# Performance work log

Measured on AMD Instinct MI355X. Metric: run time of the kernel, lower is better.

## Reference

```python
import jax, jax.numpy as jnp
import numpy as np

DIM = 2048
HEADS = 16
HEAD_DIM = 128
KV_HEADS = 8
ROPE_BASE = 10000.0


def _rope_tables(seq_len):
    inv_freq = 1.0 / (ROPE_BASE ** (jnp.arange(0, HEAD_DIM, 2, dtype=jnp.float32) / HEAD_DIM))
    t = jnp.arange(seq_len, dtype=jnp.float32)
    freqs = jnp.outer(t, inv_freq)              # [S, D/2]
    emb = jnp.concatenate([freqs, freqs], -1)    # [S, D]
    return jnp.cos(emb), jnp.sin(emb)


def _rotate_half(x):
    x1, x2 = jnp.split(x, 2, axis=-1)
    return jnp.concatenate([-x2, x1], axis=-1)


def setup_inputs() -> dict:
    key = jax.random.key(0)
    ks = jax.random.split(key, 5)
    B, S = 2, 2048
    s = 0.02
    return {
        "x": jax.random.normal(ks[0], (B, S, DIM), jnp.float32),
        "Wq": jax.random.normal(ks[1], (DIM, HEADS * HEAD_DIM), jnp.float32) * s,
        "Wk": jax.random.normal(ks[2], (DIM, KV_HEADS * HEAD_DIM), jnp.float32) * s,
        "Wv": jax.random.normal(ks[3], (DIM, KV_HEADS * HEAD_DIM), jnp.float32) * s,
        "Wo": jax.random.normal(ks[4], (HEADS * HEAD_DIM, DIM), jnp.float32) * s,
    }


def reference(x, Wq, Wk, Wv, Wo):
    B, S, _ = x.shape
    scale = 1.0 / np.sqrt(HEAD_DIM).astype(np.float32)
    q = (x @ Wq).reshape(B, S, HEADS, HEAD_DIM)
    k = (x @ Wk).reshape(B, S, KV_HEADS, HEAD_DIM)
    v = (x @ Wv).reshape(B, S, KV_HEADS, HEAD_DIM)
    cos, sin = _rope_tables(S)                   # [S, D]
    cos = cos[None, :, None, :]                  # broadcast over batch, heads
    sin = sin[None, :, None, :]
    q = q * cos + _rotate_half(q) * sin
    k = k * cos + _rotate_half(k) * sin
    q = jnp.transpose(q, (0, 2, 1, 3))           # [B,H,S,D]
    k = jnp.transpose(k, (0, 2, 1, 3))           # [B,Hkv,S,D]
    v = jnp.transpose(v, (0, 2, 1, 3))
    rep = HEADS // KV_HEADS
    k = jnp.repeat(k, rep, axis=1)               # GQA -> [B,H,S,D]
    v = jnp.repeat(v, rep, axis=1)
    scores = jnp.einsum('bhid,bhjd->bhij', q, k) * scale
    causal = jnp.tril(jnp.ones((S, S), dtype=bool))
    scores = jnp.where(causal, scores, -jnp.inf)
    attn = jax.nn.softmax(scores, axis=-1)
    out = jnp.einsum('bhij,bhjd->bhid', attn, v)
    out = jnp.transpose(out, (0, 2, 1, 3)).reshape(B, S, HEADS * HEAD_DIM)
    return out @ Wo
```

## Files before the change

### kernel.cpp

```cpp
#include <hip/hip_runtime.h>

#define DIMX 2048
#define SEQ  2048
#define BATCH 2
#define NH   16
#define NKV  8
#define HD   128
#define MTOK (BATCH*SEQ)
#define NQKV 4096
#define QKLD 3072

typedef __bf16 bf16x8 __attribute__((ext_vector_type(8)));
typedef float  f32x4  __attribute__((ext_vector_type(4)));
typedef float  f32x16 __attribute__((ext_vector_type(16)));
typedef unsigned short u16x8 __attribute__((ext_vector_type(8)));
typedef unsigned short u16x4 __attribute__((ext_vector_type(4)));
typedef unsigned int   u32x4 __attribute__((ext_vector_type(4)));

__device__ __forceinline__ unsigned short f2bf(float f) {
    unsigned u = __builtin_bit_cast(unsigned, f);
    u += 0x7fffu + ((u >> 16) & 1u);
    return (unsigned short)(u >> 16);
}
__device__ __forceinline__ float bf2f(unsigned short h) {
    unsigned u = ((unsigned)h) << 16;
    return __builtin_bit_cast(float, u);
}

__device__ __forceinline__ void gload16(const void* g, void* l) {
    __builtin_amdgcn_global_load_lds(
        (const __attribute__((address_space(1))) unsigned int*)g,
        (__attribute__((address_space(3))) unsigned int*)l, 16, 0, 0);
}

__global__ __launch_bounds__(256) void k_convert(const float* __restrict__ in,
                                                 unsigned short* __restrict__ out, int n8) {
    int i = blockIdx.x * 256 + threadIdx.x;
    if (i >= n8) return;
    f32x4 a = ((const f32x4*)in)[(size_t)i*2];
    f32x4 b = ((const f32x4*)in)[(size_t)i*2+1];
    u16x8 o;
    o[0]=f2bf(a[0]); o[1]=f2bf(a[1]); o[2]=f2bf(a[2]); o[3]=f2bf(a[3]);
    o[4]=f2bf(b[0]); o[5]=f2bf(b[1]); o[6]=f2bf(b[2]); o[7]=f2bf(b[3]);
    ((u16x8*)out)[i] = o;
}

__global__ __launch_bounds__(256) void k_transpose(const float* __restrict__ W,
                                                   unsigned short* __restrict__ Wt,
                                                   int K, int N) {
    __shared__ unsigned short tile[64*65];
    int t = threadIdx.x;
    int n0 = blockIdx.x * 64, k0 = blockIdx.y * 64;
    #pragma unroll
    for (int i = 0; i < 16; ++i) {
        int idx = t + i*256, r = idx >> 6, c = idx & 63;
        tile[r*65+c] = f2bf(W[(size_t)(k0+r)*N + n0 + c]);
    }
    __syncthreads();
    #pragma unroll
    for (int i = 0; i < 16; ++i) {
        int idx = t + i*256, n = idx >> 6, k = idx & 63;
        Wt[(size_t)(n0+n)*K + k0 + k] = tile[k*65+n];
    }
}

template<int NREP, int MODE>
__global__ __launch_bounds__(512, 2) void k_gemm256(const unsigned short* __restrict__ A,
                                                    const unsigned short* __restrict__ Bt,
                                                    void* __restrict__ Cv,
                                                    unsigned short* __restrict__ Vt,
                                                    int M, int N, int K, int ldc) {
    constexpr int BN  = NREP * 64;
    constexpr int BWC = NREP * 16;
    __shared__ __align__(16) char As[2][32768];
    __shared__ __align__(16) char Bs[2][BN * 128];
    int bid = blockIdx.x;
    int rem = (bid & 7) * 32 + (bid >> 3);
    int bx = rem & 15, by = rem >> 4;
    int row0 = by * 256, col0 = bx * BN;
    int tid = threadIdx.x, wave = tid >> 6, lane = tid & 63;
    int wr = wave >> 2, wc = wave & 3;
    int g = lane >> 4, r16 = lane & 15;
    const char* Ab = (const char*)A;
    const char* Bb = (const char*)Bt;

    f32x4 acc[8][NREP] = {};

    auto STAGE = [&](int buf, int t) {
        int k0b = t * 128;
        #pragma unroll
        for (int p = 0; p < 4; ++p) {
            int c = wave * 4 + p;
            int o = c * 1024 + lane * 16;
            int row = o >> 7;
            int colb = (o & 127) ^ ((row & 7) << 4);
            gload16(Ab + (size_t)(row0 + row) * (size_t)(K * 2) + k0b + colb, &As[buf][c * 1024]);
        }
        #pragma unroll
        for (int p = 0; p < NREP; ++p) {
            int c = wave * NREP + p;
            int o = c * 1024 + lane * 16;
            int row = o >> 7;
            int colb = (o & 127) ^ ((row & 7) << 4);
            gload16(Bb + (size_t)(col0 + row) * (size_t)(K * 2) + k0b + colb, &Bs[buf][c * 1024]);
        }
    };

    int nt = K >> 6;
    STAGE(0, 0);
    STAGE(1, 1);
    if constexpr (NREP == 4) asm volatile("s_waitcnt vmcnt(8)" ::: "memory");
    else                     asm volatile("s_waitcnt vmcnt(6)" ::: "memory");
    __builtin_amdgcn_s_barrier();

    for (int t = 0; t < nt; ++t) {
        int buf = t & 1;
        const char* AL = As[buf];
        const char* BL = Bs[buf];
        bf16x8 a0[4][2], a1[4][2], bfr[NREP][2];
        #pragma unroll
        for (int mi = 0; mi < 4; ++mi)
            #pragma unroll
            for (int s = 0; s < 2; ++s) {
                int r = wr*128 + mi*16 + r16;
                int o = r*128 + s*64 + g*16;
                a0[mi][s] = *(const bf16x8*)(AL + (o ^ ((r & 7) << 4)));
            }
        #pragma unroll
        for (int ni = 0; ni < NREP; ++ni)
            #pragma unroll
            for (int s = 0; s < 2; ++s) {
                int r = wc*BWC + ni*16 + r16;
                int o = r*128 + s*64 + g*16;
                bfr[ni][s] = *(const bf16x8*)(BL + (o ^ ((r & 7) << 4)));
            }
        __builtin_amdgcn_s_setprio(1);
        #pragma unroll
        for (int mi = 0; mi < 4; ++mi)
            #pragma unroll
            for (int ni = 0; ni < NREP; ++ni)
                #pragma unroll
                for (int s = 0; s < 2; ++s)
                    acc[mi][ni] = __builtin_amdgcn_mfma_f32_16x16x32_bf16(a0[mi][s], bfr[ni][s], acc[mi][ni], 0, 0, 0);
        __builtin_amdgcn_s_setprio(0);
        #pragma unroll
        for (int mi = 0; mi < 4; ++mi)
            #pragma unroll
            for (int s = 0; s < 2; ++s) {
                int r = wr*128 + 64 + mi*16 + r16;
                int o = r*128 + s*64 + g*16;
                a1[mi][s] = *(const bf16x8*)(AL + (o ^ ((r & 7) << 4)));
            }
        asm volatile("s_waitcnt lgkmcnt(0)" ::: "memory");
        __builtin_amdgcn_sched_barrier(0);
        __builtin_amdgcn_s_barrier();
        if (t + 2 < nt) STAGE(buf, t + 2);
        __builtin_amdgcn_sched_barrier(0);
        __builtin_amdgcn_s_setprio(1);
        #pragma unroll
        for (int mi = 0; mi < 4; ++mi)
            #pragma unroll
            for (int ni = 0; ni < NREP; ++ni)
                #pragma unroll
                for (int s = 0; s < 2; ++s)
                    acc[mi+4][ni] = __builtin_amdgcn_mfma_f32_16x16x32_bf16(a1[mi][s], bfr[ni][s], acc[mi+4][ni], 0, 0, 0);
        __builtin_amdgcn_s_setprio(0);
        if (t + 2 < nt) {
            if constexpr (NREP == 4) asm volatile("s_waitcnt vmcnt(8)" ::: "memory");
            else                     asm volatile("s_waitcnt vmcnt(6)" ::: "memory");
        } else {
            asm volatile("s_waitcnt vmcnt(0)" ::: "memory");
        }
        __builtin_amdgcn_s_barrier();
    }

    #pragma unroll
    for (int mi = 0; mi < 8; ++mi)
        #pragma unroll
        for (int ni = 0; ni < NREP; ++ni) {
            if (MODE == 0 && col0 >= 3072) {
                int vcol = col0 + wc*BWC + ni*16 + r16 - 3072;
                int d = vcol & 127, kh = vcol >> 7;
                int row = row0 + wr*128 + mi*16 + g*4;
                int b = row >> 11, s = row & (SEQ-1);
                u16x4 pk;
                #pragma unroll
                for (int rr = 0; rr < 4; ++rr) pk[rr] = f2bf(acc[mi][ni][rr]);
                *(u16x4*)&Vt[((size_t)(b*NKV + kh)*HD + d)*SEQ + s] = pk;
            } else {
                #pragma unroll
                for (int rr = 0; rr < 4; ++rr) {
                    int row = row0 + wr*128 + mi*16 + g*4 + rr;
                    int col = col0 + wc*BWC + ni*16 + r16;
                    float v = acc[mi][ni][rr];
                    if (MODE == 1) ((float*)Cv)[(size_t)row*ldc + col] = v;
                    else ((unsigned short*)Cv)[(size_t)row*ldc + col] = f2bf(v);
                }
            }
        }
}

__global__ __launch_bounds__(256) void k_rope(unsigned short* __restrict__ qkv) {
    int tid = blockIdx.x * 256 + threadIdx.x;
    int i    = tid & 63;
    int rest = tid >> 6;
    int head = rest % (NH + NKV);
    int tok  = rest / (NH + NKV);
    int pos  = tok & (SEQ - 1);
    size_t base = (size_t)tok * QKLD + head*HD;
    float x1 = bf2f(qkv[base + i]);
    float x2 = bf2f(qkv[base + i + 64]);
    float inv = exp2f(-0.20762050593046014f * (float)i);
    float ang = (float)pos * inv;
    float s, c;
    sincosf(ang, &s, &c);
    float sc = (head < NH) ? 0.12754984523341717f : 1.0f;
    qkv[base + i]      = f2bf((x1*c - x2*s) * sc);
    qkv[base + i + 64] = f2bf((x2*c + x1*s) * sc);
}

__global__ __launch_bounds__(256, 2) void k_attn(const unsigned short* __restrict__ qkv,
                                                 const unsigned short* __restrict__ Vt,
                                                 unsigned short* __restrict__ attn_out) {
    __shared__ __align__(16) char KVs[2][32768];
    int bid = blockIdx.x;
    int half = bid >> 8;
    int rem  = bid & 255;
    int xcd = rem & 7, idx = rem >> 3;
    int bh  = xcd * 4 + (idx >> 3);
    int p   = idx & 7;
    int qt  = half ? (15 - p) : p;
    int b = bh >> 4, h = bh & 15, kvh = h >> 1;
    int tid = threadIdx.x, wave = tid >> 6, lane = tid & 63;
    int l31 = lane & 31, hi = lane >> 5;
    int nt = 2*qt + 2;
    int q0w = qt*128 + wave*32;
    int qg  = q0w + l31;
    const unsigned short* qbase = qkv + (size_t)(b*SEQ)*QKLD;
    const char* kbase = (const char*)(qbase + DIMX + kvh*HD);
    const char* vbase = (const char*)(Vt + ((size_t)(b*NKV + kvh)*HD)*SEQ);

    bf16x8 qf[8];
    {
        const unsigned short* qr = qbase + (size_t)qg*QKLD + h*HD;
        #pragma unroll
        for (int s2 = 0; s2 < 8; ++s2) qf[s2] = *(const bf16x8*)(qr + s2*16 + hi*8);
    }

    f32x16 acc[4] = {};
    float mrow = -1e30f, lrow = 0.f;

    auto STAGE = [&](int v, int buf) {
        int kv0 = v * 64;
        char* KL = KVs[buf];
        char* VL = KL + 16384;
        #pragma unroll
        for (int pp = 0; pp < 4; ++pp) {
            int c = wave*4 + pp;
            int row  = c*4 + (lane >> 4);
            int colb = ((lane & 15) * 16) ^ ((row & 7) << 4);
            gload16(kbase + (size_t)(kv0 + row)*(QKLD*2) + colb, KL + c*1024);
            int d    = c*8 + (lane >> 3);
            int colv = ((lane & 7) * 16) ^ ((d & 7) << 4);
            gload16(vbase + (size_t)d*(SEQ*2) + (size_t)kv0*2 + colv, VL + c*1024);
        }
    };

    STAGE(0, 0);
    asm volatile("s_waitcnt vmcnt(0)" ::: "memory");
    __syncthreads();

    for (int v = 0; v < nt; ++v) {
        int buf = v & 1;
        int kv0 = v * 64;
        if (v + 1 < nt) STAGE(v + 1, buf ^ 1);
        const char* KL = KVs[buf];
        const char* VL = KL + 16384;
        if (kv0 <= q0w + 31) {
            f32x16 st0 = {}, st1 = {};
            const char* kr0 = KL + l31*256;
            const char* kr1 = KL + (32 + l31)*256;
            unsigned sw = (unsigned)((l31 & 7) << 4);
            __builtin_amdgcn_s_setprio(1);
            #pragma unroll
            for (int s2 = 0; s2 < 8; ++s2) {
                unsigned off = (unsigned)(s2*32 + hi*16);
                bf16x8 kf0 = *(const bf16x8*)(kr0 + (off ^ sw));
                bf16x8 kf1 = *(const bf16x8*)(kr1 + (off ^ sw));
                st0 = __builtin_amdgcn_mfma_f32_32x32x16_bf16(kf0, qf[s2], st0, 0, 0, 0);
                st1 = __builtin_amdgcn_mfma_f32_32x32x16_bf16(kf1, qf[s2], st1, 0, 0, 0);
            }
            __builtin_amdgcn_s_setprio(0);
            if (kv0 + 63 > q0w) {
                #pragma unroll
                for (int r = 0; r < 16; ++r) {
                    int kvr = kv0 + (r & 3) + 8*(r >> 2) + 4*hi;
                    st0[r] = (kvr      <= qg) ? st0[r] : -1e30f;
                    st1[r] = (kvr + 32 <= qg) ? st1[r] : -1e30f;
                }
            }
            float mt = -1e30f;
            #pragma unroll
            for (int r = 0; r < 16; ++r) { mt = fmaxf(mt, st0[r]); mt = fmaxf(mt, st1[r]); }
            mt = fmaxf(mt, __shfl_xor(mt, 32, 64));
            if (!__all(mt - mrow <= 8.0f)) {
                float mn = fmaxf(mrow, mt);
                float corr = exp2f(mrow - mn);
                mrow = mn; lrow *= corr;
                #pragma unroll
                for (int dt = 0; dt < 4; ++dt)
                    #pragma unroll
                    for (int r = 0; r < 16; ++r) acc[dt][r] *= corr;
            }
            float rs = 0.f;
            #pragma unroll
            for (int r = 0; r < 16; ++r) {
                float p0 = exp2f(st0[r] - mrow); st0[r] = p0; rs += p0;
                float p1 = exp2f(st1[r] - mrow); st1[r] = p1; rs += p1;
            }
            lrow += rs + __shfl_xor(rs, 32, 64);
            #pragma unroll
            for (int t = 0; t < 2; ++t)
                #pragma unroll
                for (int ks = 0; ks < 2; ++ks) {
                    const f32x16& stt = t ? st1 : st0;
                    int rb = ks * 8;
                    float p0 = stt[rb+0], p1 = stt[rb+1], p2 = stt[rb+2], p3 = stt[rb+3];
                    float p4 = stt[rb+4], p5 = stt[rb+5], p6 = stt[rb+6], p7 = stt[rb+7];
                    unsigned w0, w1, w2, w3;
                    asm("v_cvt_pk_bf16_f32 %0, %1, %2" : "=v"(w0) : "v"(p0), "v"(p1));
                    asm("v_cvt_pk_bf16_f32 %0, %1, %2" : "=v"(w1) : "v"(p2), "v"(p3));
                    asm("v_cvt_pk_bf16_f32 %0, %1, %2" : "=v"(w2) : "v"(p4), "v"(p5));
                    asm("v_cvt_pk_bf16_f32 %0, %1, %2" : "=v"(w3) : "v"(p6), "v"(p7));
                    asm("v_permlane32_swap_b32 %0, %1" : "+v"(w0), "+v"(w2));
                    asm("v_permlane32_swap_b32 %0, %1" : "+v"(w1), "+v"(w3));
                    u32x4 pu = {w0, w1, w2, w3};
                    bf16x8 pfrag = __builtin_bit_cast(bf16x8, pu);
                    int ks4 = t*2 + ks;
                    __builtin_amdgcn_s_setprio(1);
                    #pragma unroll
                    for (int dt = 0; dt < 4; ++dt) {
                        int d = dt*32 + l31;
                        bf16x8 vf = *(const bf16x8*)(VL + d*128 +
                                     (((unsigned)(ks4*32 + hi*16)) ^ ((unsigned)((d & 7) << 4))));
                        acc[dt] = __builtin_amdgcn_mfma_f32_32x32x16_bf16(vf, pfrag, acc[dt], 0, 0, 0);
                    }
                    __builtin_amdgcn_s_setprio(0);
                }
        }
        asm volatile("s_waitcnt vmcnt(0)" ::: "memory");
        __syncthreads();
    }

    float inv = 1.0f / lrow;
    #pragma unroll
    for (int dt = 0; dt < 4; ++dt)
        #pragma unroll
        for (int qd = 0; qd < 4; ++qd) {
            u16x4 o4;
            #pragma unroll
            for (int j = 0; j < 4; ++j) o4[j] = f2bf(acc[dt][qd*4 + j] * inv);
            *(u16x4*)&attn_out[(size_t)(b*SEQ + qg)*DIMX + h*HD + dt*32 + qd*8 + hi*4] = o4;
        }
}

extern "C" void kernel_launch(void* const* d_in, const int* in_sizes, int n_in,
                              void* d_out, int out_size, void* d_ws, size_t ws_size,
                              hipStream_t stream) {
    const float* x  = (const float*)d_in[0];
    const float* Wq = (const float*)d_in[1];
    const float* Wk = (const float*)d_in[2];
    const float* Wv = (const float*)d_in[3];
    const float* Wo = (const float*)d_in[4];

    unsigned short* xb   = (unsigned short*)d_ws;
    unsigned short* Wtq  = xb  + (size_t)MTOK*DIMX;
    unsigned short* Wto  = Wtq + (size_t)NQKV*DIMX;
    unsigned short* qkv  = Wto + (size_t)DIMX*DIMX;
    unsigned short* aout = qkv + (size_t)MTOK*QKLD;
    unsigned short* Vt   = aout + (size_t)MTOK*DIMX;

    k_convert<<<(MTOK*DIMX/8 + 255)/256, 256, 0, stream>>>(x, xb, MTOK*DIMX/8);

    dim3 tg32(DIMX/64, DIMX/64);
    dim3 tg16(1024/64, DIMX/64);
    k_transpose<<<tg32, 256, 0, stream>>>(Wq, Wtq,                         DIMX, DIMX);
    k_transpose<<<tg16, 256, 0, stream>>>(Wk, Wtq + (size_t)2048*DIMX,     DIMX, 1024);
    k_transpose<<<tg16, 256, 0, stream>>>(Wv, Wtq + (size_t)3072*DIMX,     DIMX, 1024);
    k_transpose<<<tg32, 256, 0, stream>>>(Wo, Wto,                         DIMX, DIMX);

    k_gemm256<4, 0><<<256, 512, 0, stream>>>(xb, Wtq, qkv, Vt, MTOK, NQKV, DIMX, QKLD);

    k_rope<<<(MTOK*(NH+NKV)*64)/256, 256, 0, stream>>>(qkv);

    k_attn<<<512, 256, 0, stream>>>(qkv, Vt, aout);

    k_gemm256<2, 1><<<256, 512, 0, stream>>>(aout, Wto, (float*)d_out, nullptr, MTOK, DIMX, DIMX, DIMX);
}
```

Before: 215.8 us.

## Add 8-phase pipelined 256x256 GEMM kernel for QKV projection

Adds a new GEMM kernel that splits each K-step into four MFMA phases over half-tiles of A and B. Global-to-LDS loads for the next steps are interleaved between the phases, with explicit barriers and waitcnts and raised wave priority around the MFMA blocks. The aim is to overlap memory traffic with matrix math better than the previous double-buffered kernel. The QKV projection now uses it, while the output projection keeps the old kernel. The extra barriers add synchronisation cost, and the hand-tuned vmcnt counts are fragile.

```diff
diff --git a/kernel.cpp b/kernel.cpp
--- a/kernel.cpp
+++ b/kernel.cpp
@@ -62,6 +62,154 @@
         int idx = t + i*256, n = idx >> 6, k = idx & 63;
         Wt[(size_t)(n0+n)*K + k0 + k] = tile[k*65+n];
     }
+}
+
+template<int MODE>
+__global__ __launch_bounds__(512, 2) void k_gemm8p(const unsigned short* __restrict__ A,
+                                                   const unsigned short* __restrict__ Bt,
+                                                   void* __restrict__ Cv,
+                                                   unsigned short* __restrict__ Vt,
+                                                   int M, int N, int K, int ldc) {
+    __shared__ __align__(16) char LA[2][32768];
+    __shared__ __align__(16) char LB[2][32768];
+    int bid = blockIdx.x;
+    int rem = (bid & 7) * 32 + (bid >> 3);
+    int bx = rem & 15, by = rem >> 4;
+    int row0 = by * 256, col0 = bx * 256;
+    int tid = threadIdx.x, wave = tid >> 6, lane = tid & 63;
+    int wr = wave >> 2, wc = wave & 3;
+    int g = lane >> 4, r16 = lane & 15;
+    const char* Ab = (const char*)A;
+    const char* Bb = (const char*)Bt;
+
+    f32x4 acc[8][4] = {};
+    bf16x8 af[4][2], bf[4][2];
+
+    int l8 = lane >> 3;
+    int colb = ((lane & 7) * 16) ^ (l8 << 4);
+
+    auto stageA = [&](int buf, int hf, int step) {
+        int k0b = step << 7;
+        #pragma unroll
+        for (int j = 0; j < 2; ++j) {
+            int c = wave * 2 + j;
+            int block = c >> 3, sub = c & 7;
+            int rbase = block*128 + hf*64 + sub*8;
+            gload16(Ab + (size_t)(row0 + rbase + l8) * (size_t)(K * 2) + k0b + colb,
+                    LA[buf] + block*16384 + hf*8192 + sub*1024);
+        }
+    };
+    auto stageB = [&](int buf, int hf, int step) {
+        int k0b = step << 7;
+        #pragma unroll
+        for (int j = 0; j < 2; ++j) {
+            int c = wave * 2 + j;
+            int block = c >> 2, sub = c & 3;
+            int rbase = block*64 + hf*32 + sub*8;
+            gload16(Bb + (size_t)(col0 + rbase + l8) * (size_t)(K * 2) + k0b + colb,
+                    LB[buf] + block*8192 + hf*4096 + sub*1024);
+        }
+    };
+    auto readA = [&](const char* AL, int hf) {
+        #pragma unroll
+        for (int mi = 0; mi < 4; ++mi)
+            #pragma unroll
+            for (int s = 0; s < 2; ++s) {
+                int r = wr*128 + hf*64 + mi*16 + r16;
+                int o = r*128 + s*64 + g*16;
+                af[mi][s] = *(const bf16x8*)(AL + (o ^ ((r & 7) << 4)));
+            }
+    };
+    auto readB = [&](const char* BL, int cp) {
+        #pragma unroll
+        for (int n2 = 0; n2 < 2; ++n2)
+            #pragma unroll
+            for (int s = 0; s < 2; ++s) {
+                int ni = cp*2 + n2;
+                int r = wc*64 + ni*16 + r16;
+                int o = r*128 + s*64 + g*16;
+                bf[ni][s] = *(const bf16x8*)(BL + (o ^ ((r & 7) << 4)));
+            }
+    };
+    auto MF = [&](int hf, int cp) {
+        __builtin_amdgcn_s_setprio(1);
+        #pragma unroll
+        for (int mi = 0; mi < 4; ++mi)
+            #pragma unroll
+            for (int n2 = 0; n2 < 2; ++n2)
+                #pragma unroll
+                for (int s = 0; s < 2; ++s)
+                    acc[hf*4+mi][cp*2+n2] = __builtin_amdgcn_mfma_f32_16x16x32_bf16(
+                        af[mi][s], bf[cp*2+n2][s], acc[hf*4+mi][cp*2+n2], 0, 0, 0);
+        __builtin_amdgcn_s_setprio(0);
+    };
+
+    int nsteps = K >> 6;
+    stageA(0,0,0); stageA(0,1,0); stageB(0,0,0); stageB(0,1,0);
+    stageA(1,0,1); stageB(1,1,1); stageA(1,1,1);
+    asm volatile("s_waitcnt vmcnt(6)" ::: "memory");
+    __builtin_amdgcn_s_barrier();
+
+    for (int t = 0; t < nsteps; ++t) {
+        int buf = t & 1, pb = buf ^ 1;
+        const char* AL = LA[buf];
+        const char* BL = LB[buf];
+        bool s1 = (t + 1 < nsteps), s2 = (t + 2 < nsteps);
+        readA(AL, 0); readB(BL, 0);
+        if (s1) stageB(pb, 0, t+1);
+        __builtin_amdgcn_s_barrier();
+        asm volatile("s_waitcnt lgkmcnt(0)" ::: "memory");
+        __builtin_amdgcn_sched_barrier(0);
+        MF(0, 0);
+        __builtin_amdgcn_s_barrier();
+        readB(BL, 1);
+        if (s2) stageA(buf, 0, t+2);
+        __builtin_amdgcn_s_barrier();
+        asm volatile("s_waitcnt lgkmcnt(0)" ::: "memory");
+        __builtin_amdgcn_sched_barrier(0);
+        MF(0, 1);
+        __builtin_amdgcn_s_barrier();
+        readA(AL, 1);
+        if (s2) stageB(buf, 1, t+2);
+        __builtin_amdgcn_s_barrier();
+        asm volatile("s_waitcnt lgkmcnt(0)" ::: "memory");
+        __builtin_amdgcn_sched_barrier(0);
+        MF(1, 1);
+        __builtin_amdgcn_s_barrier();
+        if (s2) stageA(buf, 1, t+2);
+        __builtin_amdgcn_s_barrier();
+        asm volatile("s_waitcnt lgkmcnt(0)" ::: "memory");
+        __builtin_amdgcn_sched_barrier(0);
+        MF(1, 0);
+        if (s2) { asm volatile("s_waitcnt vmcnt(6)" ::: "memory"); }
+        else    { asm volatile("s_waitcnt vmcnt(0)" ::: "memory"); }
+        __builtin_amdgcn_s_barrier();
+    }
+
+    #pragma unroll
+    for (int mi = 0; mi < 8; ++mi)
+        #pragma unroll
+        for (int ni = 0; ni < 4; ++ni) {
+            if (MODE == 0 && col0 >= 3072) {
+                int vcol = col0 + wc*64 + ni*16 + r16 - 3072;
+                int d = vcol & 127, kh = vcol >> 7;
+                int row = row0 + wr*128 + mi*16 + g*4;
+                int b = row >> 11, s = row & (SEQ-1);
+                u16x4 pk;
+                #pragma unroll
+                for (int rr = 0; rr < 4; ++rr) pk[rr] = f2bf(acc[mi][ni][rr]);
+                *(u16x4*)&Vt[((size_t)(b*NKV + kh)*HD + d)*SEQ + s] = pk;
+            } else {
+                #pragma unroll
+                for (int rr = 0; rr < 4; ++rr) {
+                    int row = row0 + wr*128 + mi*16 + g*4 + rr;
+                    int col = col0 + wc*64 + ni*16 + r16;
+                    float v = acc[mi][ni][rr];
+                    if (MODE == 1) ((float*)Cv)[(size_t)row*ldc + col] = v;
+                    else ((unsigned short*)Cv)[(size_t)row*ldc + col] = f2bf(v);
+                }
+            }
+        }
 }
 
 template<int NREP, int MODE>
@@ -389,7 +537,7 @@
     k_transpose<<<tg16, 256, 0, stream>>>(Wv, Wtq + (size_t)3072*DIMX,     DIMX, 1024);
     k_transpose<<<tg32, 256, 0, stream>>>(Wo, Wto,                         DIMX, DIMX);
 
-    k_gemm256<4, 0><<<256, 512, 0, stream>>>(xb, Wtq, qkv, Vt, MTOK, NQKV, DIMX, QKLD);
+    k_gemm8p<0><<<256, 512, 0, stream>>>(xb, Wtq, qkv, Vt, MTOK, NQKV, DIMX, QKLD);
 
     k_rope<<<(MTOK*(NH+NKV)*64)/256, 256, 0, stream>>>(qkv);
 
```

After: 219.7 us. No clear change (+1.8%).

## Split long causal query tiles across two blocks with flag-based partial merge

Applied to the files above, without the earlier changes.

The eight longest query tiles per head are split along the KV range into two blocks. Each block writes bf16 partial accumulators plus row max and sum to workspace, and the second block to finish, found via an atomic counter, merges both and writes the output. The grid grows from 512 to 768 blocks to even out per-block work and reduce tail imbalance from the causal mask. The cost is extra partial traffic, a memset, and some bf16 rounding of partials; flags and partials reuse existing workspace regions that are already consumed (xb, and the tail of Wtq just before Wto).

```diff
diff --git a/kernel.cpp b/kernel.cpp
--- a/kernel.cpp
+++ b/kernel.cpp
@@ -221,19 +221,24 @@
 
 __global__ __launch_bounds__(256, 2) void k_attn(const unsigned short* __restrict__ qkv,
                                                  const unsigned short* __restrict__ Vt,
-                                                 unsigned short* __restrict__ attn_out) {
+                                                 unsigned short* __restrict__ attn_out,
+                                                 char* __restrict__ partials,
+                                                 int* __restrict__ flags) {
     __shared__ __align__(16) char KVs[2][32768];
+    __shared__ int oldFlag;
     int bid = blockIdx.x;
-    int half = bid >> 8;
-    int rem  = bid & 255;
-    int xcd = rem & 7, idx = rem >> 3;
-    int bh  = xcd * 4 + (idx >> 3);
-    int p   = idx & 7;
-    int qt  = half ? (15 - p) : p;
+    int xcd = bid & 7, slot = bid >> 3;
+    int grp = slot / 24, s24 = slot % 24;
+    int bh  = xcd * 4 + grp;
+    int qt, ks; bool split;
+    if (s24 < 16) { split = true;  qt = 15 - (s24 >> 1); ks = s24 & 1; }
+    else          { split = false; qt = 23 - s24;        ks = 0;       }
     int b = bh >> 4, h = bh & 15, kvh = h >> 1;
     int tid = threadIdx.x, wave = tid >> 6, lane = tid & 63;
     int l31 = lane & 31, hi = lane >> 5;
-    int nt = 2*qt + 2;
+    int ntf = 2*qt + 2;
+    int vbeg = (split && ks) ? (ntf >> 1) : 0;
+    int vend = (split && !ks) ? (ntf >> 1) : ntf;
     int q0w = qt*128 + wave*32;
     int qg  = q0w + l31;
     const unsigned short* qbase = qkv + (size_t)(b*SEQ)*QKLD;
@@ -266,14 +271,14 @@
         }
     };
 
-    STAGE(0, 0);
+    STAGE(vbeg, vbeg & 1);
     asm volatile("s_waitcnt vmcnt(0)" ::: "memory");
     __syncthreads();
 
-    for (int v = 0; v < nt; ++v) {
+    for (int v = vbeg; v < vend; ++v) {
         int buf = v & 1;
         int kv0 = v * 64;
-        if (v + 1 < nt) STAGE(v + 1, buf ^ 1);
+        if (v + 1 < vend) STAGE(v + 1, buf ^ 1);
         const char* KL = KVs[buf];
         const char* VL = KL + 16384;
         if (kv0 <= q0w + 31) {
@@ -322,9 +327,9 @@
             #pragma unroll
             for (int t = 0; t < 2; ++t)
                 #pragma unroll
-                for (int ks = 0; ks < 2; ++ks) {
+                for (int ks2 = 0; ks2 < 2; ++ks2) {
                     const f32x16& stt = t ? st1 : st0;
-                    int rb = ks * 8;
+                    int rb = ks2 * 8;
                     float p0 = stt[rb+0], p1 = stt[rb+1], p2 = stt[rb+2], p3 = stt[rb+3];
                     float p4 = stt[rb+4], p5 = stt[rb+5], p6 = stt[rb+6], p7 = stt[rb+7];
                     unsigned w0, w1, w2, w3;
@@ -336,7 +341,7 @@
                     asm("v_permlane32_swap_b32 %0, %1" : "+v"(w1), "+v"(w3));
                     u32x4 pu = {w0, w1, w2, w3};
                     bf16x8 pfrag = __builtin_bit_cast(bf16x8, pu);
-                    int ks4 = t*2 + ks;
+                    int ks4 = t*2 + ks2;
                     __builtin_amdgcn_s_setprio(1);
                     #pragma unroll
                     for (int dt = 0; dt < 4; ++dt) {
@@ -352,14 +357,67 @@
         __syncthreads();
     }
 
-    float inv = 1.0f / lrow;
+    int qw = wave*32 + l31;
+    if (!split) {
+        float inv = 1.0f / lrow;
+        #pragma unroll
+        for (int dt = 0; dt < 4; ++dt)
+            #pragma unroll
+            for (int qd = 0; qd < 4; ++qd) {
+                u16x4 o4;
+                #pragma unroll
+                for (int j = 0; j < 4; ++j) o4[j] = f2bf(acc[dt][qd*4 + j] * inv);
+                *(u16x4*)&attn_out[(size_t)(b*SEQ + qg)*DIMX + h*HD + dt*32 + qd*8 + hi*4] = o4;
+            }
+        return;
+    }
+
+    int pairIdx = bh*8 + (qt - 8);
+    constexpr int SLOT = 33792;
+    char* mySlot = partials + (size_t)(pairIdx*2 + ks) * SLOT;
+    {
+        unsigned short* pacc = (unsigned short*)mySlot;
+        #pragma unroll
+        for (int dt = 0; dt < 4; ++dt)
+            #pragma unroll
+            for (int qd = 0; qd < 4; ++qd) {
+                u16x4 pk;
+                #pragma unroll
+                for (int j = 0; j < 4; ++j) pk[j] = f2bf(acc[dt][qd*4 + j]);
+                *(u16x4*)&pacc[qw*128 + dt*32 + qd*8 + hi*4] = pk;
+            }
+        if (hi == 0) {
+            ((float*)(mySlot + 32768))[qw] = mrow;
+            ((float*)(mySlot + 33280))[qw] = lrow;
+        }
+    }
+    __threadfence();
+    __syncthreads();
+    if (tid == 0) oldFlag = atomicAdd(&flags[pairIdx], 1);
+    __syncthreads();
+    if (oldFlag == 0) return;
+    __threadfence();
+
+    const char* pSlot = partials + (size_t)(pairIdx*2 + (ks ^ 1)) * SLOT;
+    const unsigned short* pacc = (const unsigned short*)pSlot;
+    float mp = ((const float*)(pSlot + 32768))[qw];
+    float lp = ((const float*)(pSlot + 33280))[qw];
+    float nm = fmaxf(mrow, mp);
+    float ssf = exp2f(mrow - nm);
+    float spf = exp2f(mp   - nm);
+    float lm  = lrow*ssf + lp*spf;
+    float invl = 1.0f / lm;
     #pragma unroll
     for (int dt = 0; dt < 4; ++dt)
         #pragma unroll
         for (int qd = 0; qd < 4; ++qd) {
+            u16x4 pp = *(const u16x4*)&pacc[qw*128 + dt*32 + qd*8 + hi*4];
             u16x4 o4;
             #pragma unroll
-            for (int j = 0; j < 4; ++j) o4[j] = f2bf(acc[dt][qd*4 + j] * inv);
+            for (int j = 0; j < 4; ++j) {
+                float v = bf2f(f2bf(acc[dt][qd*4 + j]))*ssf + bf2f(pp[j])*spf;
+                o4[j] = f2bf(v * invl);
+            }
             *(u16x4*)&attn_out[(size_t)(b*SEQ + qg)*DIMX + h*HD + dt*32 + qd*8 + hi*4] = o4;
         }
 }
@@ -379,6 +437,8 @@
     unsigned short* qkv  = Wto + (size_t)DIMX*DIMX;
     unsigned short* aout = qkv + (size_t)MTOK*QKLD;
     unsigned short* Vt   = aout + (size_t)MTOK*DIMX;
+    char* partials = (char*)xb;
+    int*  flags    = (int*)Wto - 256;
 
     k_convert<<<(MTOK*DIMX/8 + 255)/256, 256, 0, stream>>>(x, xb, MTOK*DIMX/8);
 
@@ -393,7 +453,8 @@
 
     k_rope<<<(MTOK*(NH+NKV)*64)/256, 256, 0, stream>>>(qkv);
 
-    k_attn<<<512, 256, 0, stream>>>(qkv, Vt, aout);
+    hipMemsetAsync(flags, 0, 256 * sizeof(int), stream);
+    k_attn<<<768, 256, 0, stream>>>(qkv, Vt, aout, partials, flags);
 
     k_gemm256<2, 1><<<256, 512, 0, stream>>>(aout, Wto, (float*)d_out, nullptr, MTOK, DIMX, DIMX, DIMX);
 }
```

Measured after the change: 327.9 us. 52.0% more time.
